# Optimization experiments

Hardware: AMD Instinct MI355X
Metric: run time of the kernel (lower is better)

## Reference

```python
import jax, jax.numpy as jnp
import numpy as np

B, F, E, A, T, H = 16384, 1024, 28, 2, 128, 4
HD = T // H  # head dim = 32

def _ln(x, g, b, eps=1e-5):
    m = jnp.mean(x, axis=-1, keepdims=True)
    v = jnp.var(x, axis=-1, keepdims=True)
    return (x - m) / jnp.sqrt(v + eps) * g + b

def _gelu(x):
    return jax.nn.gelu(x, approximate=False)  # torch nn.GELU default (erf)

def setup_inputs() -> dict:
    key = jax.random.key(0)
    ks = iter(jax.random.split(key, 48))
    def rn(shape, s=0.02):
        return jax.random.normal(next(ks), shape, jnp.float32) * s
    d = dict(
        fusion_feat=jax.random.normal(next(ks), (B, F), jnp.float32),
        explicit_logits=jax.random.normal(next(ks), (B, E), jnp.float32),
        implicit_logits=jax.random.normal(next(ks), (B, E), jnp.float32),
        affect_vec=jax.random.normal(next(ks), (B, A), jnp.float32),
        ln_exp_g=jnp.ones((E,), jnp.float32), ln_exp_b=jnp.zeros((E,), jnp.float32),
        W_exp=rn((E, T)), b_exp=jnp.zeros((T,), jnp.float32),
        ln_imp_g=jnp.ones((E,), jnp.float32), ln_imp_b=jnp.zeros((E,), jnp.float32),
        W_imp=rn((E, T)), b_imp=jnp.zeros((T,), jnp.float32),
        ln_aff_g=jnp.ones((A,), jnp.float32), ln_aff_b=jnp.zeros((A,), jnp.float32),
        W_aff=rn((A, T)), b_aff=jnp.zeros((T,), jnp.float32),
        Wq_in=rn((F, T)), bq_in=jnp.zeros((T,), jnp.float32),   # query_proj
        Wq=rn((T, T)), bq=jnp.zeros((T,), jnp.float32),         # MHA in_proj q
        Wk=rn((T, T)), bk=jnp.zeros((T,), jnp.float32),         # MHA in_proj k
        Wv=rn((T, T)), bv=jnp.zeros((T,), jnp.float32),         # MHA in_proj v
        Wo=rn((T, T)), bo=jnp.zeros((T,), jnp.float32),         # MHA out_proj
        Wc=rn((T, F)), bc=jnp.zeros((F,), jnp.float32),         # context_proj
        Ws=rn((3 * T, F)), bs=jnp.zeros((F,), jnp.float32),     # summary_proj
        Wg1=rn((2 * F, F)), bg1=jnp.zeros((F,), jnp.float32),   # gate layer 1
        Wg2=rn((F, F)), bg2=jnp.zeros((F,), jnp.float32),       # gate layer 2
        ln_out_g=jnp.ones((F,), jnp.float32), ln_out_b=jnp.zeros((F,), jnp.float32),
    )
    return d

def reference(fusion_feat, explicit_logits, implicit_logits, affect_vec,
              ln_exp_g, ln_exp_b, W_exp, b_exp,
              ln_imp_g, ln_imp_b, W_imp, b_imp,
              ln_aff_g, ln_aff_b, W_aff, b_aff,
              Wq_in, bq_in, Wq, bq, Wk, bk, Wv, bv, Wo, bo,
              Wc, bc, Ws, bs, Wg1, bg1, Wg2, bg2, ln_out_g, ln_out_b):
    p_exp = jax.nn.softmax(explicit_logits, axis=-1)
    p_imp = jax.nn.softmax(implicit_logits, axis=-1)
    exp_e = _gelu(_ln(p_exp, ln_exp_g, ln_exp_b) @ W_exp + b_exp)       # (B,T)
    imp_e = _gelu(_ln(p_imp, ln_imp_g, ln_imp_b) @ W_imp + b_imp)       # (B,T)
    aff_e = _gelu(_ln(affect_vec, ln_aff_g, ln_aff_b) @ W_aff + b_aff)  # (B,T)
    tokens = jnp.stack([exp_e, imp_e, aff_e], axis=1)                   # (B,3,T)
    q = fusion_feat @ Wq_in + bq_in                                     # (B,T)
    # tiny 1-query x 3-key multi-head cross attention (dropout=eval/identity)
    qh = (q @ Wq + bq).reshape(B, H, HD)
    kh = (tokens @ Wk + bk).reshape(B, 3, H, HD)
    vh = (tokens @ Wv + bv).reshape(B, 3, H, HD)
    scores = jnp.einsum('bhd,bshd->bhs', qh, kh) / np.float32(np.sqrt(HD))
    w = jax.nn.softmax(scores, axis=-1)                                 # (B,H,3)
    attn_weights = jnp.mean(w, axis=1)                                  # avg heads -> (B,3)
    attn_out = jnp.einsum('bhs,bshd->bhd', w, vh).reshape(B, T) @ Wo + bo
    context = attn_out @ Wc + bc                                        # (B,F)
    gate_h = _gelu(jnp.concatenate([fusion_feat, context], axis=-1) @ Wg1 + bg1)
    gate = jax.nn.sigmoid(gate_h @ Wg2 + bg2)
    refined = _ln(fusion_feat + gate * context, ln_out_g, ln_out_b)
    summary = _gelu(jnp.concatenate([exp_e, imp_e, aff_e], axis=-1) @ Ws + bs)
    return refined, attn_weights, summary
```

## Files before the change

kernel.cpp:

```cpp
#include <hip/hip_runtime.h>
#include <hip/hip_bf16.h>
#include <stdint.h>


using bf16 = __hip_bfloat16;
typedef __bf16 bf16x8 __attribute__((ext_vector_type(8)));
typedef float f32x4 __attribute__((ext_vector_type(4)));

__device__ __forceinline__ float b2f(bf16 x) { return __bfloat162float(x); }
__device__ __forceinline__ bf16 f2b(float x) { return __float2bfloat16(x); }

__device__ __forceinline__ float fast_tanh(float y) {
  float z = fabsf(y);
  float t = __expf(-2.f * z);
  float r = (1.f - t) / (1.f + t);
  return copysignf(r, y);
}
__device__ __forceinline__ float gelu_f(float x) {
  return 0.5f * x * (1.f + fast_tanh(0.7978845608028654f * (x + 0.044715f * x * x * x)));
}
__device__ __forceinline__ float sigmoid_f(float v) {
  return 1.f / (1.f + __expf(-v));
}

__device__ __forceinline__ void async_ld16(const void* g, void* l) {
  using GP = const __attribute__((address_space(1))) uint32_t*;
  using LP = __attribute__((address_space(3))) uint32_t*;
  __builtin_amdgcn_global_load_lds((GP)g, (LP)l, 16, 0, 0);
}

template <int EPI, typename OutT, int MT>
__device__ __forceinline__ void gemm128_dev(
    int bx, int by,
    const bf16* A0, const bf16* A1, int ksplit, int lda0, int lda1,
    const bf16* __restrict__ BT, int K,
    const float* __restrict__ bias,
    OutT* out, int ldo,
    const bf16* ffp, const bf16* ctxp, int ldfc)
{
  constexpr int MIC = MT / 32;
  __shared__ uint16_t smA[MT * 64];
  __shared__ uint16_t smB[128 * 64];
  const int tid = threadIdx.x;
  const int w = tid >> 6;
  const int l = tid & 63;
  const int m0 = bx * MT;
  const int n0 = by * 128;
  const int wr = w >> 1, wc = w & 1;
  const int lrow = l & 15, lquad = l >> 4;
  const int rb = w * 8 + (l >> 3);
  const int cpos = l & 7;

  const f32x4 vzero = {0.f, 0.f, 0.f, 0.f};
  f32x4 acc[MIC][4];
#pragma unroll
  for (int i = 0; i < MIC; i++)
#pragma unroll
    for (int j = 0; j < 4; j++) acc[i][j] = vzero;

  for (int k0 = 0; k0 < K; k0 += 64) {
    __syncthreads();
#pragma unroll
    for (int i = 0; i < MIC; i++) {
      int row = i * 32 + rb;
      int cg = cpos ^ (row & 7);
      int kcol = k0 + cg * 8;
      const bf16* gp = (kcol < ksplit)
                           ? (A0 + (size_t)(m0 + row) * lda0 + kcol)
                           : (A1 + (size_t)(m0 + row) * lda1 + (kcol - ksplit));
      async_ld16(gp, &smA[(i * 32 + w * 8) * 64]);
    }
#pragma unroll
    for (int i = 0; i < 4; i++) {
      int row = i * 32 + rb;
      int cg = cpos ^ (row & 7);
      const bf16* gq = BT + (size_t)(n0 + row) * K + k0 + cg * 8;
      async_ld16(gq, &smB[(i * 32 + w * 8) * 64]);
    }
    __syncthreads();
#pragma unroll
    for (int kk = 0; kk < 2; kk++) {
      bf16x8 af[MIC], bfr[4];
      const int cc = kk * 4 + lquad;
#pragma unroll
      for (int mi = 0; mi < MIC; mi++) {
        int r = wr * (MT / 2) + mi * 16 + lrow;
        af[mi] = *(const bf16x8*)&smA[r * 64 + ((cc ^ (r & 7)) << 3)];
      }
#pragma unroll
      for (int ni = 0; ni < 4; ni++) {
        int r = wc * 64 + ni * 16 + lrow;
        bfr[ni] = *(const bf16x8*)&smB[r * 64 + ((cc ^ (r & 7)) << 3)];
      }
#pragma unroll
      for (int mi = 0; mi < MIC; mi++)
#pragma unroll
        for (int ni = 0; ni < 4; ni++)
          acc[mi][ni] =
              __builtin_amdgcn_mfma_f32_16x16x32_bf16(af[mi], bfr[ni], acc[mi][ni], 0, 0, 0);
    }
  }

#pragma unroll
  for (int mi = 0; mi < MIC; mi++) {
#pragma unroll
    for (int ni = 0; ni < 4; ni++) {
#pragma unroll
      for (int r = 0; r < 4; r++) {
        int row = m0 + wr * (MT / 2) + mi * 16 + lquad * 4 + r;
        int col = n0 + wc * 64 + ni * 16 + lrow;
        float v = acc[mi][ni][r] + (bias ? bias[col] : 0.f);
        if (EPI == 1) v = gelu_f(v);
        if (EPI == 2) {
          float gate = sigmoid_f(v);
          size_t fo = (size_t)row * ldfc + col;
          v = b2f(ffp[fo]) + gate * b2f(ctxp[fo]);
        }
        if constexpr (__is_same(OutT, float))
          out[(size_t)row * ldo + col] = v;
        else
          out[(size_t)row * ldo + col] = f2b(v);
      }
    }
  }
}

template <int EPI, typename OutT, int MT>
__launch_bounds__(256)
__global__ void gemm128_k(const bf16* A0, const bf16* A1, int ksplit, int lda0, int lda1,
                          const bf16* __restrict__ BT, int K,
                          const float* __restrict__ bias,
                          OutT* out, int ldo,
                          const bf16* ffp, const bf16* ctxp, int ldfc)
{
  gemm128_dev<EPI, OutT, MT>(blockIdx.x, blockIdx.y, A0, A1, ksplit, lda0, lda1,
                             BT, K, bias, out, ldo, ffp, ctxp, ldfc);
}

__launch_bounds__(256)
__global__ void folds_k(const bf16* WQT, const bf16* WQINB, bf16* WQQT,
                        const bf16* WCT, const bf16* WOB, bf16* WOCT)
{
  int bid = blockIdx.x;
  if (bid < 8) {
    gemm128_dev<0, bf16, 128>(0, bid, WQT, WQT, 128, 128, 128, WQINB, 128,
                              nullptr, WQQT, 1024, nullptr, nullptr, 0);
  } else {
    gemm128_dev<0, bf16, 128>(bid - 8, 0, WCT, WCT, 128, 128, 128, WOB, 128,
                              nullptr, WOCT, 128, nullptr, nullptr, 0);
  }
}

__launch_bounds__(256)
__global__ void g12_k(const bf16* FFB, const bf16* WQQT, const float* BQQ, bf16* QH,
                      const bf16* TOK, const bf16* WKVT, const float* BKV, bf16* KVH)
{
  int bid = blockIdx.x;
  if (bid < 768) {
    gemm128_dev<0, bf16, 128>(bid % 384, bid / 384, TOK, TOK, 128, 128, 128,
                              WKVT, 128, BKV, KVH, 256, nullptr, nullptr, 0);
  } else {
    gemm128_dev<0, bf16, 128>(bid - 768, 0, FFB, FFB, 1024, 1024, 1024,
                              WQQT, 1024, BQQ, QH, 128, nullptr, nullptr, 0);
  }
}

template <int EPI, typename OutT>
__launch_bounds__(512, 2)
__global__ void gemm256(const bf16* A0, const bf16* A1, int ksplit, int lda0, int lda1,
                        const bf16* __restrict__ BT, int K,
                        const float* __restrict__ bias,
                        OutT* out, int ldo,
                        const bf16* ffp, const bf16* ctxp, int ldfc)
{
  __shared__ uint16_t smA[2][256 * 64];
  __shared__ uint16_t smB[2][256 * 64];
  const int tid = threadIdx.x;
  const int w = tid >> 6;
  const int l = tid & 63;
  const int m0 = blockIdx.x * 256;
  const int n0 = blockIdx.y * 256;
  const int wr = w >> 2;
  const int wc = w & 3;
  const int lrow = l & 15, lquad = l >> 4;
  const int rb = tid >> 3;
  const int cpos = tid & 7;
  const int NT = K >> 6;

  const f32x4 vzero = {0.f, 0.f, 0.f, 0.f};
  f32x4 acc[8][4];
#pragma unroll
  for (int mi = 0; mi < 8; mi++)
#pragma unroll
    for (int ni = 0; ni < 4; ni++) acc[mi][ni] = vzero;

  auto stage = [&](int buf, int tt) {
    const int k0 = tt << 6;
    const bf16* Ab; int la, kc;
    if (k0 < ksplit) { Ab = A0; la = lda0; kc = k0; }
    else             { Ab = A1; la = lda1; kc = k0 - ksplit; }
#pragma unroll
    for (int i = 0; i < 4; i++) {
      const int row = i * 64 + rb;
      const int cg = cpos ^ (row & 7);
      async_ld16(Ab + (size_t)(m0 + row) * la + kc + cg * 8,
                 &smA[buf][(i * 64 + w * 8) * 64]);
    }
#pragma unroll
    for (int i = 0; i < 4; i++) {
      const int row = i * 64 + rb;
      const int cg = cpos ^ (row & 7);
      async_ld16(BT + (size_t)(n0 + row) * K + k0 + cg * 8,
                 &smB[buf][(i * 64 + w * 8) * 64]);
    }
  };

  int cur = 0;

  auto readfrags = [&](int kk, bf16x8 (&af)[8], bf16x8 (&bfr)[4]) {
    const int cc = kk * 4 + lquad;
#pragma unroll
    for (int mi = 0; mi < 8; mi++) {
      int r = wr * 128 + mi * 16 + lrow;
      af[mi] = *(const bf16x8*)&smA[cur][r * 64 + (((cc) ^ (r & 7)) << 3)];
    }
#pragma unroll
    for (int ni = 0; ni < 4; ni++) {
      int r = wc * 64 + ni * 16 + lrow;
      bfr[ni] = *(const bf16x8*)&smB[cur][r * 64 + (((cc) ^ (r & 7)) << 3)];
    }
  };
  auto domfma = [&](bf16x8 (&af)[8], bf16x8 (&bfr)[4]) {
#pragma unroll
    for (int mi = 0; mi < 8; mi++)
#pragma unroll
      for (int ni = 0; ni < 4; ni++)
        acc[mi][ni] =
            __builtin_amdgcn_mfma_f32_16x16x32_bf16(af[mi], bfr[ni], acc[mi][ni], 0, 0, 0);
  };

  stage(0, 0);
  stage(1, 1);
  asm volatile("s_waitcnt vmcnt(8)" ::: "memory");
  __builtin_amdgcn_s_barrier();
  __builtin_amdgcn_sched_barrier(0);

  for (int t = 0; t < NT; ++t) {
    bf16x8 af[8], bfr[4];
    readfrags(0, af, bfr);
    __builtin_amdgcn_s_setprio(1);
    domfma(af, bfr);
    __builtin_amdgcn_s_setprio(0);
    readfrags(1, af, bfr);
    asm volatile("s_waitcnt lgkmcnt(0)" ::: "memory");
    __builtin_amdgcn_s_barrier();
    __builtin_amdgcn_sched_barrier(0);
    if (t + 2 < NT) stage(cur, t + 2);
    __builtin_amdgcn_s_setprio(1);
    domfma(af, bfr);
    __builtin_amdgcn_s_setprio(0);
    if (t + 2 < NT) {
      asm volatile("s_waitcnt vmcnt(8)" ::: "memory");
    } else {
      asm volatile("s_waitcnt vmcnt(0)" ::: "memory");
    }
    __builtin_amdgcn_s_barrier();
    __builtin_amdgcn_sched_barrier(0);
    cur ^= 1;
  }

#pragma unroll
  for (int mi = 0; mi < 8; mi++) {
#pragma unroll
    for (int ni = 0; ni < 4; ni++) {
#pragma unroll
      for (int r = 0; r < 4; r++) {
        int row = m0 + wr * 128 + mi * 16 + lquad * 4 + r;
        int col = n0 + wc * 64 + ni * 16 + lrow;
        float v = acc[mi][ni][r] + (bias ? bias[col] : 0.f);
        if (EPI == 1) v = gelu_f(v);
        if (EPI == 2) {
          float gate = sigmoid_f(v);
          size_t fo = (size_t)row * ldfc + col;
          v = b2f(ffp[fo]) + gate * b2f(ctxp[fo]);
        }
        if constexpr (__is_same(OutT, float))
          out[(size_t)row * ldo + col] = v;
        else
          out[(size_t)row * ldo + col] = f2b(v);
      }
    }
  }
}

__device__ __forceinline__ void emb28_256(const float* __restrict__ logits,
                                          const float* __restrict__ g,
                                          const float* __restrict__ bb,
                                          const float* __restrict__ W,
                                          const float* __restrict__ wb,
                                          bf16* __restrict__ out, int t,
                                          float* sv, float* sp)
{
  if (t < 28) sv[t] = logits[t];
  __syncthreads();
  float mx = sv[0];
#pragma unroll
  for (int e = 1; e < 28; e++) mx = fmaxf(mx, sv[e]);
  if (t < 28) sp[t] = __expf(sv[t] - mx);
  __syncthreads();
  float sum = 0.f;
#pragma unroll
  for (int e = 0; e < 28; e++) sum += sp[e];
  float inv = 1.f / sum;
  float sp2 = 0.f;
#pragma unroll
  for (int e = 0; e < 28; e++) { float p = sp[e] * inv; sp2 += p * p; }
  const float mean = 1.f / 28.f;
  float var = sp2 * (1.f / 28.f) - mean * mean;
  float rstd = rsqrtf(var + 1e-5f);
  __syncthreads();
  if (t < 28) sp[t] = (sp[t] * inv - mean) * rstd * g[t] + bb[t];
  __syncthreads();
  if (t < 128) {
    float acc = wb[t];
#pragma unroll
    for (int e = 0; e < 28; e++) acc += sp[e] * W[e * 128 + t];
    out[t] = f2b(gelu_f(acc));
  }
  __syncthreads();
}

__global__ void preamble(
    const float* __restrict__ ff, bf16* __restrict__ FFB,
    const float* __restrict__ exl, const float* __restrict__ iml, const float* __restrict__ affv,
    const float* __restrict__ geg, const float* __restrict__ geb,
    const float* __restrict__ Wex, const float* __restrict__ bex,
    const float* __restrict__ gig, const float* __restrict__ gib,
    const float* __restrict__ Wim, const float* __restrict__ bim,
    const float* __restrict__ gag, const float* __restrict__ gab,
    const float* __restrict__ Waf, const float* __restrict__ baf,
    bf16* __restrict__ TOK,
    const float* __restrict__ Wq, const float* __restrict__ Wc,
    const float* __restrict__ Ws, const float* __restrict__ Wg1,
    const float* __restrict__ Wg2,
    bf16* WQT, bf16* WCT, bf16* WST, bf16* WG1T, bf16* WG2T,
    const float* __restrict__ Wk, const float* __restrict__ bk,
    const float* __restrict__ Wv, const float* __restrict__ bv,
    const float* __restrict__ Wq_in, const float* __restrict__ bq_in,
    const float* __restrict__ bq, const float* __restrict__ Wo,
    const float* __restrict__ bo, const float* __restrict__ bc,
    bf16* WKVT, float* BKV, float* BQQ, float* BOC, bf16* WQINB, bf16* WOB)
{
  __shared__ float tile[32][33];
  __shared__ float sv[28], sp[28];
  int bid = blockIdx.x;
  const int t = threadIdx.x;

  if (bid < 16384) {
    size_t i = (size_t)bid * 1024 + (size_t)t * 4;
    float4 v = *reinterpret_cast<const float4*>(ff + i);
    ushort4 o;
    o.x = __builtin_bit_cast(unsigned short, f2b(v.x));
    o.y = __builtin_bit_cast(unsigned short, f2b(v.y));
    o.z = __builtin_bit_cast(unsigned short, f2b(v.z));
    o.w = __builtin_bit_cast(unsigned short, f2b(v.w));
    *reinterpret_cast<ushort4*>(FFB + i) = o;
    bf16* trow = TOK + (size_t)bid * 384;
    emb28_256(exl + (size_t)bid * 28, geg, geb, Wex, bex, trow, t, sv, sp);
    emb28_256(iml + (size_t)bid * 28, gig, gib, Wim, bim, trow + 128, t, sv, sp);
    if (t < 128) {
      float a0 = affv[(size_t)bid * 2 + 0];
      float a1 = affv[(size_t)bid * 2 + 1];
      float m = 0.5f * (a0 + a1);
      float d0 = a0 - m, d1 = a1 - m;
      float var = 0.5f * (d0 * d0 + d1 * d1);
      float rstd = rsqrtf(var + 1e-5f);
      float l0 = d0 * rstd * gag[0] + gab[0];
      float l1 = d1 * rstd * gag[1] + gab[1];
      float acc = baf[t] + l0 * Waf[t] + l1 * Waf[128 + t];
      trow[256 + t] = f2b(gelu_f(acc));
    }
    return;
  }
  bid -= 16384;
  if (bid < 3600) {
    const float* in; bf16* outp; int R, C, bx, by;
    if (bid < 16)                 { in = Wq;  outp = WQT;  R = 128;  C = 128;  bx = bid & 3;  by = bid >> 2; }
    else if ((bid -= 16) < 128)   { in = Wc;  outp = WCT;  R = 128;  C = 1024; bx = bid & 31; by = bid >> 5; }
    else if ((bid -= 128) < 384)  { in = Ws;  outp = WST;  R = 384;  C = 1024; bx = bid & 31; by = bid >> 5; }
    else if ((bid -= 384) < 2048) { in = Wg1; outp = WG1T; R = 2048; C = 1024; bx = bid & 31; by = bid >> 5; }
    else { bid -= 2048;             in = Wg2; outp = WG2T; R = 1024; C = 1024; bx = bid & 31; by = bid >> 5; }
    const int tx = t & 31, ty = t >> 5;
    const int c0 = bx * 32, r0 = by * 32;
#pragma unroll
    for (int i = 0; i < 4; i++) {
      int r = ty + i * 8;
      tile[r][tx] = in[(size_t)(r0 + r) * C + c0 + tx];
    }
    __syncthreads();
#pragma unroll
    for (int i = 0; i < 4; i++) {
      int c = ty + i * 8;
      outp[(size_t)(c0 + c) * R + r0 + tx] = f2b(tile[tx][c]);
    }
    return;
  }
  bid -= 3600;
  int idx = bid * 256 + t;
  if (idx < 32768) {
    int n = idx >> 7, k = idx & 127;
    WKVT[idx] = f2b((n < 128) ? Wk[k * 128 + n] : Wv[k * 128 + (n - 128)]);
    return;
  }
  idx -= 32768;
  if (idx < 256) { BKV[idx] = (idx < 128) ? bk[idx] : bv[idx - 128]; return; }
  idx -= 256;
  if (idx < 128) {
    float s = bq[idx];
    for (int u = 0; u < 128; u++) s += bq_in[u] * Wq[u * 128 + idx];
    BQQ[idx] = s;
    return;
  }
  idx -= 128;
  if (idx < 1024) {
    float s = bc[idx];
    for (int u = 0; u < 128; u++) s += bo[u] * Wc[u * 1024 + idx];
    BOC[idx] = s;
    return;
  }
  idx -= 1024;
  if (idx < 131072) { WQINB[idx] = f2b(Wq_in[idx]); return; }
  idx -= 131072;
  if (idx < 16384) { WOB[idx] = f2b(Wo[idx]); return; }
}

__global__ void attn_kernel(const bf16* __restrict__ qh, const bf16* __restrict__ kvh,
                            bf16* __restrict__ apre, float* __restrict__ attw)
{
  const int b = blockIdx.x, t = threadIdx.x;
  float q = b2f(qh[(size_t)b * 128 + t]);
  const bf16* kv = kvh + (size_t)b * 3 * 256;
  float s[3], v[3];
#pragma unroll
  for (int i = 0; i < 3; i++) {
    float k = b2f(kv[i * 256 + t]);
    v[i] = b2f(kv[i * 256 + 128 + t]);
    float r = q * k;
#pragma unroll
    for (int off = 16; off > 0; off >>= 1) r += __shfl_down(r, off, 32);
    r = __shfl(r, 0, 32);
    s[i] = r * 0.17677669529663687f;
  }
  float mx = fmaxf(s[0], fmaxf(s[1], s[2]));
  float e0 = __expf(s[0] - mx), e1 = __expf(s[1] - mx), e2 = __expf(s[2] - mx);
  float inv = 1.f / (e0 + e1 + e2);
  float w0 = e0 * inv, w1 = e1 * inv, w2 = e2 * inv;
  apre[(size_t)b * 128 + t] = f2b(w0 * v[0] + w1 * v[1] + w2 * v[2]);
  __shared__ float aw[4][3];
  if ((t & 31) == 0) { int h = t >> 5; aw[h][0] = w0; aw[h][1] = w1; aw[h][2] = w2; }
  __syncthreads();
  if (t < 3)
    attw[(size_t)b * 3 + t] = 0.25f * (aw[0][t] + aw[1][t] + aw[2][t] + aw[3][t]);
}

__global__ void ln_out_kernel(const bf16* __restrict__ x, const float* __restrict__ g,
                              const float* __restrict__ bb, float* __restrict__ out)
{
  const int row = blockIdx.x, t = threadIdx.x;
  const bf16* xr = x + (size_t)row * 1024;
  ushort4 u = *reinterpret_cast<const ushort4*>(xr + t * 4);
  float v0 = __uint_as_float((uint32_t)u.x << 16);
  float v1 = __uint_as_float((uint32_t)u.y << 16);
  float v2 = __uint_as_float((uint32_t)u.z << 16);
  float v3 = __uint_as_float((uint32_t)u.w << 16);
  float s = v0 + v1 + v2 + v3;
  float s2 = v0 * v0 + v1 * v1 + v2 * v2 + v3 * v3;
#pragma unroll
  for (int off = 32; off > 0; off >>= 1) {
    s += __shfl_down(s, off, 64);
    s2 += __shfl_down(s2, off, 64);
  }
  __shared__ float ls[4], ls2[4];
  const int w = t >> 6;
  if ((t & 63) == 0) { ls[w] = s; ls2[w] = s2; }
  __syncthreads();
  float S = ls[0] + ls[1] + ls[2] + ls[3];
  float S2 = ls2[0] + ls2[1] + ls2[2] + ls2[3];
  float mean = S * (1.f / 1024.f);
  float var = S2 * (1.f / 1024.f) - mean * mean;
  float rstd = rsqrtf(var + 1e-5f);
  const int c = t * 4;
  float4 o;
  o.x = (v0 - mean) * rstd * g[c + 0] + bb[c + 0];
  o.y = (v1 - mean) * rstd * g[c + 1] + bb[c + 1];
  o.z = (v2 - mean) * rstd * g[c + 2] + bb[c + 2];
  o.w = (v3 - mean) * rstd * g[c + 3] + bb[c + 3];
  *reinterpret_cast<float4*>(out + (size_t)row * 1024 + c) = o;
}

extern "C" void kernel_launch(void* const* d_in, const int* in_sizes, int n_in,
                              void* d_out, int out_size, void* d_ws, size_t ws_size,
                              hipStream_t stream)
{
  const float* ff   = (const float*)d_in[0];
  const float* exl  = (const float*)d_in[1];
  const float* iml  = (const float*)d_in[2];
  const float* affv = (const float*)d_in[3];
  const float* geg = (const float*)d_in[4],  *geb = (const float*)d_in[5];
  const float* Wex = (const float*)d_in[6],  *bex = (const float*)d_in[7];
  const float* gig = (const float*)d_in[8],  *gib = (const float*)d_in[9];
  const float* Wim = (const float*)d_in[10], *bim = (const float*)d_in[11];
  const float* gag = (const float*)d_in[12], *gab = (const float*)d_in[13];
  const float* Waf = (const float*)d_in[14], *baf = (const float*)d_in[15];
  const float* Wq_in = (const float*)d_in[16], *bq_in = (const float*)d_in[17];
  const float* Wq = (const float*)d_in[18], *bq = (const float*)d_in[19];
  const float* Wk = (const float*)d_in[20], *bk = (const float*)d_in[21];
  const float* Wv = (const float*)d_in[22], *bv = (const float*)d_in[23];
  const float* Wo = (const float*)d_in[24], *bo = (const float*)d_in[25];
  const float* Wc = (const float*)d_in[26], *bc = (const float*)d_in[27];
  const float* Ws = (const float*)d_in[28], *bs = (const float*)d_in[29];
  const float* Wg1 = (const float*)d_in[30], *bg1 = (const float*)d_in[31];
  const float* Wg2 = (const float*)d_in[32], *bg2 = (const float*)d_in[33];
  const float* lng = (const float*)d_in[34], *lnb = (const float*)d_in[35];

  char* ws = (char*)d_ws;
  bf16*  WKVT = (bf16*)(ws + 0);
  float* BKV  = (float*)(ws + 65536);
  bf16*  WQQT = (bf16*)(ws + 66560);
  float* BQQ  = (float*)(ws + 328704);
  bf16*  WOCT = (bf16*)(ws + 329216);
  float* BOC  = (float*)(ws + 591360);
  bf16*  WST  = (bf16*)(ws + 595456);
  bf16*  WG1T = (bf16*)(ws + 1381888);
  bf16*  WG2T = (bf16*)(ws + 5576192);
  bf16*  FFB  = (bf16*)(ws + 7673344);
  bf16*  PRE  = (bf16*)(ws + 7673344);
  bf16*  TOK  = (bf16*)(ws + 41227776);
  bf16*  QH   = (bf16*)(ws + 53810688);
  bf16*  APRE = (bf16*)(ws + 58004992);

  bf16* WQT   = (bf16*)(ws + 53810688);
  bf16* WOB   = (bf16*)(ws + 53810688 + 32768);
  bf16* WQINB = (bf16*)(ws + 53810688 + 65536);
  bf16* WCT   = (bf16*)(ws + 53810688 + 327680);

  float* outp = (float*)d_out;
  float* out_refined = outp;
  float* out_attw    = outp + 16777216;
  float* out_summary = outp + 16826368;
  bf16* CTX   = (bf16*)out_refined;
  bf16* KVH   = (bf16*)out_summary;
  bf16* GATEH = (bf16*)out_summary;

  preamble<<<20694, 256, 0, stream>>>(
      ff, FFB, exl, iml, affv, geg, geb, Wex, bex, gig, gib, Wim, bim,
      gag, gab, Waf, baf, TOK,
      Wq, Wc, Ws, Wg1, Wg2, WQT, WCT, WST, WG1T, WG2T,
      Wk, bk, Wv, bv, Wq_in, bq_in, bq, Wo, bo, bc,
      WKVT, BKV, BQQ, BOC, WQINB, WOB);
  folds_k<<<16, 256, 0, stream>>>(WQT, WQINB, WQQT, WCT, WOB, WOCT);
  g12_k<<<896, 256, 0, stream>>>(FFB, WQQT, BQQ, QH, TOK, WKVT, BKV, KVH);
  attn_kernel<<<16384, 128, 0, stream>>>(QH, KVH, APRE, out_attw);
  gemm128_k<0, bf16, 128><<<dim3(128, 8), 256, 0, stream>>>(APRE, APRE, 128, 128, 128, WOCT, 128,
                                                            BOC, CTX, 1024, nullptr, nullptr, 0);
  gemm256<1, bf16><<<dim3(64, 4), 512, 0, stream>>>(FFB, CTX, 1024, 1024, 1024, WG1T, 2048,
                                                    bg1, GATEH, 1024, nullptr, nullptr, 0);
  gemm256<2, bf16><<<dim3(64, 4), 512, 0, stream>>>(GATEH, GATEH, 1024, 1024, 1024, WG2T, 1024,
                                                    bg2, PRE, 1024, FFB, CTX, 1024);
  gemm256<1, float><<<dim3(64, 4), 512, 0, stream>>>(TOK, TOK, 384, 384, 384, WST, 384,
                                                     bs, out_summary, 1024, nullptr, nullptr, 0);
  ln_out_kernel<<<16384, 256, 0, stream>>>(PRE, lng, lnb, out_refined);
}
```

Measured before the change: 568.8 us.

## Fold context projection into gate GEMM weights and merge independent GEMM launches

The context half of the first gate GEMM (K=1024 over CTX) is replaced by a K=128 contraction over the attention pre-output. It uses folded weights Wo·Wc·Wg1 and a folded bias computed at setup, so the gate GEMM's K drops from 2048 to 1152 and it no longer depends on CTX. Independent GEMMs are then co-launched: the gate GEMM runs alongside the CTX GEMM, and the second gate GEMM runs alongside the summary GEMM, through a shared-memory device function. This cuts launches and tail idle time. The cost is extra folding GEMMs, a serial bias-fold loop, extra bf16 rounding from the weight folding, and scratch buffers placed inside the output region.

```diff
diff --git a/kernel.cpp b/kernel.cpp
--- a/kernel.cpp
+++ b/kernel.cpp
@@ -125,61 +125,21 @@
   }
 }
 
-template <int EPI, typename OutT, int MT>
-__launch_bounds__(256)
-__global__ void gemm128_k(const bf16* A0, const bf16* A1, int ksplit, int lda0, int lda1,
-                          const bf16* __restrict__ BT, int K,
-                          const float* __restrict__ bias,
-                          OutT* out, int ldo,
-                          const bf16* ffp, const bf16* ctxp, int ldfc)
-{
-  gemm128_dev<EPI, OutT, MT>(blockIdx.x, blockIdx.y, A0, A1, ksplit, lda0, lda1,
-                             BT, K, bias, out, ldo, ffp, ctxp, ldfc);
-}
-
-__launch_bounds__(256)
-__global__ void folds_k(const bf16* WQT, const bf16* WQINB, bf16* WQQT,
-                        const bf16* WCT, const bf16* WOB, bf16* WOCT)
-{
-  int bid = blockIdx.x;
-  if (bid < 8) {
-    gemm128_dev<0, bf16, 128>(0, bid, WQT, WQT, 128, 128, 128, WQINB, 128,
-                              nullptr, WQQT, 1024, nullptr, nullptr, 0);
-  } else {
-    gemm128_dev<0, bf16, 128>(bid - 8, 0, WCT, WCT, 128, 128, 128, WOB, 128,
-                              nullptr, WOCT, 128, nullptr, nullptr, 0);
-  }
-}
-
-__launch_bounds__(256)
-__global__ void g12_k(const bf16* FFB, const bf16* WQQT, const float* BQQ, bf16* QH,
-                      const bf16* TOK, const bf16* WKVT, const float* BKV, bf16* KVH)
-{
-  int bid = blockIdx.x;
-  if (bid < 768) {
-    gemm128_dev<0, bf16, 128>(bid % 384, bid / 384, TOK, TOK, 128, 128, 128,
-                              WKVT, 128, BKV, KVH, 256, nullptr, nullptr, 0);
-  } else {
-    gemm128_dev<0, bf16, 128>(bid - 768, 0, FFB, FFB, 1024, 1024, 1024,
-                              WQQT, 1024, BQQ, QH, 128, nullptr, nullptr, 0);
-  }
-}
-
 template <int EPI, typename OutT>
-__launch_bounds__(512, 2)
-__global__ void gemm256(const bf16* A0, const bf16* A1, int ksplit, int lda0, int lda1,
-                        const bf16* __restrict__ BT, int K,
-                        const float* __restrict__ bias,
-                        OutT* out, int ldo,
-                        const bf16* ffp, const bf16* ctxp, int ldfc)
-{
-  __shared__ uint16_t smA[2][256 * 64];
-  __shared__ uint16_t smB[2][256 * 64];
+__device__ __forceinline__ void gemm256_dev(
+    uint16_t* __restrict__ smem, int bx, int by,
+    const bf16* A0, const bf16* A1, int ksplit, int lda0, int lda1,
+    const bf16* B0, const bf16* B1, int bsplit, int ldb0, int ldb1,
+    int K,
+    const float* __restrict__ bias,
+    OutT* out, int ldo,
+    const bf16* ffp, const bf16* ctxp, int ldfc)
+{
   const int tid = threadIdx.x;
   const int w = tid >> 6;
   const int l = tid & 63;
-  const int m0 = blockIdx.x * 256;
-  const int n0 = blockIdx.y * 256;
+  const int m0 = bx * 256;
+  const int n0 = by * 256;
   const int wr = w >> 2;
   const int wc = w & 3;
   const int lrow = l & 15, lquad = l >> 4;
@@ -199,35 +159,42 @@
     const bf16* Ab; int la, kc;
     if (k0 < ksplit) { Ab = A0; la = lda0; kc = k0; }
     else             { Ab = A1; la = lda1; kc = k0 - ksplit; }
+    uint16_t* sA = smem + buf * 16384;
 #pragma unroll
     for (int i = 0; i < 4; i++) {
       const int row = i * 64 + rb;
       const int cg = cpos ^ (row & 7);
       async_ld16(Ab + (size_t)(m0 + row) * la + kc + cg * 8,
-                 &smA[buf][(i * 64 + w * 8) * 64]);
-    }
+                 &sA[(i * 64 + w * 8) * 64]);
+    }
+    const bf16* Bb; int lb, kb;
+    if (k0 < bsplit) { Bb = B0; lb = ldb0; kb = k0; }
+    else             { Bb = B1; lb = ldb1; kb = k0 - bsplit; }
+    uint16_t* sB = smem + 32768 + buf * 16384;
 #pragma unroll
     for (int i = 0; i < 4; i++) {
       const int row = i * 64 + rb;
       const int cg = cpos ^ (row & 7);
-      async_ld16(BT + (size_t)(n0 + row) * K + k0 + cg * 8,
-                 &smB[buf][(i * 64 + w * 8) * 64]);
+      async_ld16(Bb + (size_t)(n0 + row) * lb + kb + cg * 8,
+                 &sB[(i * 64 + w * 8) * 64]);
     }
   };
 
   int cur = 0;
 
   auto readfrags = [&](int kk, bf16x8 (&af)[8], bf16x8 (&bfr)[4]) {
+    const uint16_t* sA = smem + cur * 16384;
+    const uint16_t* sB = smem + 32768 + cur * 16384;
     const int cc = kk * 4 + lquad;
 #pragma unroll
     for (int mi = 0; mi < 8; mi++) {
       int r = wr * 128 + mi * 16 + lrow;
-      af[mi] = *(const bf16x8*)&smA[cur][r * 64 + (((cc) ^ (r & 7)) << 3)];
+      af[mi] = *(const bf16x8*)&sA[r * 64 + ((cc ^ (r & 7)) << 3)];
     }
 #pragma unroll
     for (int ni = 0; ni < 4; ni++) {
       int r = wc * 64 + ni * 16 + lrow;
-      bfr[ni] = *(const bf16x8*)&smB[cur][r * 64 + (((cc) ^ (r & 7)) << 3)];
+      bfr[ni] = *(const bf16x8*)&sB[r * 64 + ((cc ^ (r & 7)) << 3)];
     }
   };
   auto domfma = [&](bf16x8 (&af)[8], bf16x8 (&bfr)[4]) {
@@ -290,6 +257,91 @@
           out[(size_t)row * ldo + col] = f2b(v);
       }
     }
+  }
+}
+
+__launch_bounds__(512, 2)
+__global__ void big5_k(const bf16* FFB, const bf16* APRE,
+                       const bf16* WG1T, const bf16* WFOLD, const float* BG1F,
+                       bf16* GATEH,
+                       const bf16* WOCT, const float* BOC, bf16* CTX)
+{
+  __shared__ uint16_t smem[65536];
+  int bid = blockIdx.x;
+  if (bid < 256) {
+    gemm256_dev<1, bf16>(smem, bid & 63, bid >> 6,
+                         FFB, APRE, 1024, 1024, 128,
+                         WG1T, WFOLD, 1024, 2048, 128,
+                         1152, BG1F, GATEH, 1024, nullptr, nullptr, 0);
+  } else {
+    bid -= 256;
+    gemm256_dev<0, bf16>(smem, bid & 63, bid >> 6,
+                         APRE, APRE, 128, 128, 128,
+                         WOCT, WOCT, 128, 128, 128,
+                         128, BOC, CTX, 1024, nullptr, nullptr, 0);
+  }
+}
+
+__launch_bounds__(512, 2)
+__global__ void big6_k(const bf16* GATEH, const bf16* WG2T, const float* bg2,
+                       bf16* PRE, const bf16* FFB, const bf16* CTX,
+                       const bf16* TOK, const bf16* WST, const float* bs, float* SUMM)
+{
+  __shared__ uint16_t smem[65536];
+  int bid = blockIdx.x;
+  if (bid < 256) {
+    gemm256_dev<2, bf16>(smem, bid & 63, bid >> 6,
+                         GATEH, GATEH, 1024, 1024, 1024,
+                         WG2T, WG2T, 1024, 1024, 1024,
+                         1024, bg2, PRE, 1024, FFB, CTX, 1024);
+  } else {
+    bid -= 256;
+    gemm256_dev<1, float>(smem, bid & 63, bid >> 6,
+                          TOK, TOK, 384, 384, 384,
+                          WST, WST, 384, 384, 384,
+                          384, bs, SUMM, 1024, nullptr, nullptr, 0);
+  }
+}
+
+__launch_bounds__(256)
+__global__ void folds_a(const bf16* WQT, const bf16* WQINB, bf16* WQQT,
+                        const bf16* WCT, const bf16* WOB, bf16* WOCT, bf16* WOC,
+                        const float* __restrict__ Wg1, const float* __restrict__ BOC,
+                        const float* __restrict__ bg1, float* BG1F)
+{
+  int bid = blockIdx.x;
+  if (bid < 8) {
+    gemm128_dev<0, bf16, 128>(0, bid, WQT, WQT, 128, 128, 128, WQINB, 128,
+                              nullptr, WQQT, 1024, nullptr, nullptr, 0);
+  } else if (bid < 16) {
+    gemm128_dev<0, bf16, 128>(bid - 8, 0, WCT, WCT, 128, 128, 128, WOB, 128,
+                              nullptr, WOCT, 128, nullptr, nullptr, 0);
+  } else if (bid < 24) {
+    gemm128_dev<0, bf16, 128>(0, bid - 16, WOB, WOB, 128, 128, 128, WCT, 128,
+                              nullptr, WOC, 1024, nullptr, nullptr, 0);
+  } else {
+    int f = (bid - 24) * 256 + threadIdx.x;
+    float s = bg1[f];
+    for (int c = 0; c < 1024; c++) s += BOC[c] * Wg1[(size_t)(1024 + c) * 1024 + f];
+    BG1F[f] = s;
+  }
+}
+
+__launch_bounds__(256)
+__global__ void g12_k(const bf16* FFB, const bf16* WQQT, const float* BQQ, bf16* QH,
+                      const bf16* TOK, const bf16* WKVT, const float* BKV, bf16* KVH,
+                      const bf16* WG1T, const bf16* WOC, bf16* WFOLD)
+{
+  int bid = blockIdx.x;
+  if (bid < 768) {
+    gemm128_dev<0, bf16, 128>(bid % 384, bid / 384, TOK, TOK, 128, 128, 128,
+                              WKVT, 128, BKV, KVH, 256, nullptr, nullptr, 0);
+  } else if (bid < 896) {
+    gemm128_dev<0, bf16, 128>(bid - 768, 0, FFB, FFB, 1024, 1024, 1024,
+                              WQQT, 1024, BQQ, QH, 128, nullptr, nullptr, 0);
+  } else {
+    gemm128_dev<0, bf16, 128>(bid - 896, 0, WG1T + 1024, WG1T + 1024, 2048, 2048, 2048,
+                              WOC, 1024, nullptr, WFOLD, 128, nullptr, nullptr, 0);
   }
 }
 
@@ -549,8 +601,11 @@
   float* out_attw    = outp + 16777216;
   float* out_summary = outp + 16826368;
   bf16* CTX   = (bf16*)out_refined;
+  bf16* GATEH = (bf16*)((char*)out_refined + 33554432);
   bf16* KVH   = (bf16*)out_summary;
-  bf16* GATEH = (bf16*)out_summary;
+  bf16* WOC   = (bf16*)((char*)out_summary + 33554432);
+  bf16* WFOLD = (bf16*)((char*)out_summary + 34603008);
+  float* BG1F = (float*)((char*)out_summary + 35127296);
 
   preamble<<<20694, 256, 0, stream>>>(
       ff, FFB, exl, iml, affv, geg, geb, Wex, bex, gig, gib, Wim, bim,
@@ -558,16 +613,14 @@
       Wq, Wc, Ws, Wg1, Wg2, WQT, WCT, WST, WG1T, WG2T,
       Wk, bk, Wv, bv, Wq_in, bq_in, bq, Wo, bo, bc,
       WKVT, BKV, BQQ, BOC, WQINB, WOB);
-  folds_k<<<16, 256, 0, stream>>>(WQT, WQINB, WQQT, WCT, WOB, WOCT);
-  g12_k<<<896, 256, 0, stream>>>(FFB, WQQT, BQQ, QH, TOK, WKVT, BKV, KVH);
+  folds_a<<<28, 256, 0, stream>>>(WQT, WQINB, WQQT, WCT, WOB, WOCT, WOC,
+                                  Wg1, BOC, bg1, BG1F);
+  g12_k<<<904, 256, 0, stream>>>(FFB, WQQT, BQQ, QH, TOK, WKVT, BKV, KVH,
+                                 WG1T, WOC, WFOLD);
   attn_kernel<<<16384, 128, 0, stream>>>(QH, KVH, APRE, out_attw);
-  gemm128_k<0, bf16, 128><<<dim3(128, 8), 256, 0, stream>>>(APRE, APRE, 128, 128, 128, WOCT, 128,
-                                                            BOC, CTX, 1024, nullptr, nullptr, 0);
-  gemm256<1, bf16><<<dim3(64, 4), 512, 0, stream>>>(FFB, CTX, 1024, 1024, 1024, WG1T, 2048,
-                                                    bg1, GATEH, 1024, nullptr, nullptr, 0);
-  gemm256<2, bf16><<<dim3(64, 4), 512, 0, stream>>>(GATEH, GATEH, 1024, 1024, 1024, WG2T, 1024,
-                                                    bg2, PRE, 1024, FFB, CTX, 1024);
-  gemm256<1, float><<<dim3(64, 4), 512, 0, stream>>>(TOK, TOK, 384, 384, 384, WST, 384,
-                                                     bs, out_summary, 1024, nullptr, nullptr, 0);
+  big5_k<<<512, 512, 0, stream>>>(FFB, APRE, WG1T, WFOLD, BG1F, GATEH,
+                                  WOCT, BOC, CTX);
+  big6_k<<<512, 512, 0, stream>>>(GATEH, WG2T, bg2, PRE, FFB, CTX,
+                                  TOK, WST, bs, out_summary);
   ln_out_kernel<<<16384, 256, 0, stream>>>(PRE, lng, lnb, out_refined);
 }
```

Result: no change. 576.3 us (+1.3%).
